# Kernel tuning notes

Hardware: AMD Instinct MI355X
Metric: run time of the kernel (lower is better)

The kernel has to match this reference:

```python
import jax, jax.numpy as jnp
import numpy as np

# ---- module config (from init_kwargs) ----
VOL_RANGE = np.array([-40.0, -40.0, -4.0, 40.0, 40.0, 4.0], np.float32)
VOXEL_SIZE = 0.4
GRID = tuple(int(v) for v in ((VOL_RANGE[3:] - VOL_RANGE[:3]) / VOXEL_SIZE).astype(np.int32))  # (200,200,20)
SIGMA_FACTOR = 3.0
OPACITY_THRESH = 1e-4
EPS = 1e-6
K = 8  # fixed local window per Gaussian (covers 3*sigma_max/voxel_size span)

B, N, C = 1, 25000, 8


def setup_inputs() -> dict:
    key = jax.random.key(0)
    k1, k2, k3, k4, k5 = jax.random.split(key, 5)
    lo = jnp.asarray(VOL_RANGE[:3]) + 1.0
    hi = jnp.asarray(VOL_RANGE[3:]) - 1.0
    means3d = lo + (hi - lo) * jax.random.uniform(k1, (B, N, 3), jnp.float32)
    opacities = jax.random.uniform(k2, (B, N, 1), jnp.float32)
    scales = 0.05 + 0.3 * jax.random.uniform(k3, (B, N, 3), jnp.float32)  # sigma_max=0.35m -> <=6 voxel span
    rotations = jax.random.normal(k4, (B, N, 4), jnp.float32)
    features = jax.random.normal(k5, (B, N, C), jnp.float32)
    return {"means3d": means3d, "opacities": opacities, "scales": scales,
            "rotations": rotations, "features": features}


def quat_scale_to_cov(scales, rotations):
    # matches CUDAVoxelizer._get_covariance
    q = rotations / jnp.sqrt(jnp.sum(rotations ** 2, -1, keepdims=True) + 1e-8)
    r, x, y, z = q[..., 0], q[..., 1], q[..., 2], q[..., 3]
    R = jnp.stack([
        1 - 2 * (y * y + z * z), 2 * (x * y - r * z), 2 * (x * z + r * y),
        2 * (x * y + r * z), 1 - 2 * (x * x + z * z), 2 * (y * z - r * x),
        2 * (x * z - r * y), 2 * (y * z + r * x), 1 - 2 * (x * x + y * y),
    ], axis=-1).reshape(q.shape[:-1] + (3, 3))
    L = R * scales[..., None, :]  # R @ diag(scales)
    return L @ jnp.swapaxes(L, -1, -2)


def voxelize_one(means, opac, cov, feats):
    """means [N,3], opac [N,1], cov [N,3,3], feats [N,C] -> density [X,Y,Z,1], gfeat [X,Y,Z,C]."""
    X, Y, Z = GRID
    V = X * Y * Z
    vol_min = jnp.asarray(VOL_RANGE[:3])
    vol_max = jnp.asarray(VOL_RANGE[3:])
    gmax = jnp.asarray(GRID, jnp.int32) - 1

    sigma = jnp.sqrt(jnp.diagonal(cov, axis1=-2, axis2=-1))          # [N,3]
    bmin = means - SIGMA_FACTOR * sigma
    bmax = means + SIGMA_FACTOR * sigma
    # _filter_gaussians_torch as a multiplicative mask (removed Gaussians contribute 0)
    keep = (jnp.all(bmax > vol_min, -1) & jnp.all(bmin < vol_max, -1)
            & (opac[:, 0] > OPACITY_THRESH))                          # [N]

    cov_inv = jnp.linalg.inv(cov)                                     # [N,3,3]
    bmin_s = jax.lax.stop_gradient(bmin)
    bmax_s = jax.lax.stop_gradient(bmax)
    # torch .int() truncates toward zero; clamp as in fallback
    idx_min = jnp.maximum(((bmin_s - vol_min) / VOXEL_SIZE).astype(jnp.int32), 0)     # [N,3]
    idx_max = jnp.minimum(((bmax_s - vol_min) / VOXEL_SIZE).astype(jnp.int32), gmax)  # [N,3]

    o = jnp.arange(K, dtype=jnp.int32)
    offs = jnp.stack(jnp.meshgrid(o, o, o, indexing='ij'), -1).reshape(-1, 3)  # [P,3], P=K^3
    vox = idx_min[:, None, :] + offs[None]                            # [N,P,3]
    valid = jnp.all(vox <= idx_max[:, None, :], -1)                   # [N,P]

    centers = vox.astype(jnp.float32) * VOXEL_SIZE + vol_min + 0.5 * VOXEL_SIZE
    diff = centers - means[:, None, :]                                # [N,P,3]
    maha = jnp.einsum('npi,nij,npj->np', diff, cov_inv, diff)
    contrib = opac * jnp.exp(-0.5 * maha)                             # [N,P] (opac [N,1] bcast)
    contrib = jnp.where(valid & keep[:, None], contrib, 0.0)

    flat = (vox[..., 0] * Y + vox[..., 1]) * Z + vox[..., 2]
    flat = jnp.clip(flat, 0, V - 1).reshape(-1)                       # zeroed contribs land harmlessly

    density = jnp.zeros((V,), jnp.float32).at[flat].add(contrib.reshape(-1))
    gfeat = jnp.zeros((V, C), jnp.float32).at[flat].add(
        (contrib[..., None] * feats[:, None, :]).reshape(-1, C))
    gfeat = gfeat / jnp.clip(density, EPS)[:, None]
    return density.reshape(X, Y, Z, 1), gfeat.reshape(X, Y, Z, C)


def reference(means3d, opacities, scales, rotations, features):
    cov = quat_scale_to_cov(scales.reshape(-1, 3), rotations.reshape(-1, 4))
    cov = cov.reshape(means3d.shape[0], -1, 3, 3)
    density, gfeat = jax.vmap(voxelize_one)(means3d, opacities, cov, features)
    return density, gfeat
```

## Files before the change

kernel.cpp:

```cpp
#include <hip/hip_runtime.h>

namespace {
constexpr int GX = 200, GY = 200, GZ = 20;
constexpr int NVOX = GX * GY * GZ;
constexpr float VMINX = -40.f, VMINY = -40.f, VMINZ = -4.f;
constexpr float VMAXX =  40.f, VMAXY =  40.f, VMAXZ =  4.f;
constexpr float VS    = 0.4f;
constexpr float HVS   = 0.2f;
constexpr float SIGF  = 3.0f;

constexpr int TILE   = 4;
constexpr int TX     = GX / TILE;
constexpr int TY     = GY / TILE;
constexpr int NTILES = TX * TY;
constexpr int CAP    = 128;
constexpr int PSTRIDE = 20;
}

__device__ __forceinline__ bool gauss_setup(
    const float* __restrict__ means, const float* __restrict__ opacs,
    const float* __restrict__ scales, const float* __restrict__ rots,
    int g,
    int& gx0, int& gx1, int& gy0, int& gy1, int& gz0, int& gz1,
    float& i00, float& i01, float& i02, float& i11, float& i12, float& i22,
    float& mx, float& my, float& mz, float& op)
{
    op = opacs[g];
    mx = means[3*g+0]; my = means[3*g+1]; mz = means[3*g+2];
    const float sx = scales[3*g+0], sy = scales[3*g+1], sz = scales[3*g+2];
    const float q0 = rots[4*g+0], q1 = rots[4*g+1], q2 = rots[4*g+2], q3 = rots[4*g+3];

    const float qn = sqrtf(q0*q0 + q1*q1 + q2*q2 + q3*q3 + 1e-8f);
    const float r = q0/qn, x = q1/qn, y = q2/qn, z = q3/qn;

    const float R00 = 1.f - 2.f*(y*y + z*z), R01 = 2.f*(x*y - r*z), R02 = 2.f*(x*z + r*y);
    const float R10 = 2.f*(x*y + r*z), R11 = 1.f - 2.f*(x*x + z*z), R12 = 2.f*(y*z - r*x);
    const float R20 = 2.f*(x*z - r*y), R21 = 2.f*(y*z + r*x), R22 = 1.f - 2.f*(x*x + y*y);

    const float s0 = sx*sx, s1 = sy*sy, s2 = sz*sz;
    const float c00 = R00*R00*s0 + R01*R01*s1 + R02*R02*s2;
    const float c01 = R00*R10*s0 + R01*R11*s1 + R02*R12*s2;
    const float c02 = R00*R20*s0 + R01*R21*s1 + R02*R22*s2;
    const float c11 = R10*R10*s0 + R11*R11*s1 + R12*R12*s2;
    const float c12 = R10*R20*s0 + R11*R21*s1 + R12*R22*s2;
    const float c22 = R20*R20*s0 + R21*R21*s1 + R22*R22*s2;

    const float sgx = SIGF * sqrtf(c00), sgy = SIGF * sqrtf(c11), sgz = SIGF * sqrtf(c22);
    const float bminx = mx - sgx, bminy = my - sgy, bminz = mz - sgz;
    const float bmaxx = mx + sgx, bmaxy = my + sgy, bmaxz = mz + sgz;

    const bool keep = (bmaxx > VMINX) && (bmaxy > VMINY) && (bmaxz > VMINZ)
                   && (bminx < VMAXX) && (bminy < VMAXY) && (bminz < VMAXZ)
                   && (op > 1e-4f);
    if (!keep) return false;

    gx0 = max((int)((bminx - VMINX) / VS), 0);
    gy0 = max((int)((bminy - VMINY) / VS), 0);
    gz0 = max((int)((bminz - VMINZ) / VS), 0);
    gx1 = min((int)((bmaxx - VMINX) / VS), GX - 1);
    gy1 = min((int)((bmaxy - VMINY) / VS), GY - 1);
    gz1 = min((int)((bmaxz - VMINZ) / VS), GZ - 1);
    gx1 = min(gx1, gx0 + 7);
    gy1 = min(gy1, gy0 + 7);
    gz1 = min(gz1, gz0 + 7);
    if (gx1 < gx0 || gy1 < gy0 || gz1 < gz0) return false;

    const float m00 = c11*c22 - c12*c12;
    const float m01 = c02*c12 - c01*c22;
    const float m02 = c01*c12 - c02*c11;
    const float det = c00*m00 + c01*m01 + c02*m02;
    const float id  = 1.f / det;
    i00 = m00*id; i01 = m01*id; i02 = m02*id;
    i11 = (c00*c22 - c02*c02)*id;
    i12 = (c01*c02 - c00*c12)*id;
    i22 = (c00*c11 - c01*c01)*id;
    return true;
}

__global__ __launch_bounds__(64) void voxel_bin(
    const float* __restrict__ means, const float* __restrict__ opacs,
    const float* __restrict__ scales, const float* __restrict__ rots,
    const float* __restrict__ feats,
    int* __restrict__ counts, int* __restrict__ entries,
    float* __restrict__ params, int N)
{
    const int g = blockIdx.x * blockDim.x + threadIdx.x;
    if (g >= N) return;
    int gx0, gx1, gy0, gy1, gz0, gz1;
    float i00,i01,i02,i11,i12,i22, mx,my,mz, op;
    if (!gauss_setup(means, opacs, scales, rots, g,
                     gx0,gx1,gy0,gy1,gz0,gz1, i00,i01,i02,i11,i12,i22, mx,my,mz, op))
        return;

    float* P = params + (size_t)g * PSTRIDE;
    const float4 f0 = *(const float4*)(feats + 8*g);
    const float4 f1 = *(const float4*)(feats + 8*g + 4);
    *(float4*)(P + 0)  = make_float4(i00, i01, i02, i11);
    *(float4*)(P + 4)  = make_float4(i12, i22, mx, my);
    *(float4*)(P + 8)  = make_float4(mz, op,
                                     __int_as_float(gx0 | (gy0<<8) | (gz0<<16)),
                                     __int_as_float(gx1 | (gy1<<8) | (gz1<<16)));
    *(float4*)(P + 12) = f0;
    *(float4*)(P + 16) = f1;

    const int tx0 = gx0 >> 2, tx1 = gx1 >> 2;
    const int ty0 = gy0 >> 2, ty1 = gy1 >> 2;
    for (int tx = tx0; tx <= tx1; ++tx)
        for (int ty = ty0; ty <= ty1; ++ty) {
            const int t = tx * TY + ty;
            const int slot = atomicAdd(&counts[t], 1);
            if (slot < CAP) entries[t * CAP + slot] = g;
        }
}

__global__ __launch_bounds__(64) void voxel_gather(
    const float* __restrict__ params,
    const int* __restrict__ counts, const int* __restrict__ entries,
    float* __restrict__ density, float* __restrict__ gfeat)
{
    __shared__ float gs[CAP][PSTRIDE];

    const int tile = blockIdx.x;
    const int ttx = tile / TY, tty = tile % TY;
    const int tid = threadIdx.x;
    const int cnt = min(counts[tile], CAP);

    for (int j = tid; j < cnt; j += 64) {
        const int g = entries[tile * CAP + j];
        const float* P = params + (size_t)g * PSTRIDE;
        float* G = gs[j];
        #pragma unroll
        for (int q = 0; q < 5; ++q)
            *(float4*)(G + 4*q) = *(const float4*)(P + 4*q);
    }
    __syncthreads();

    const int lx = tid & 3, ly = (tid >> 2) & 3, zs = (tid >> 4) * 5;
    const int vx = ttx * TILE + lx, vy = tty * TILE + ly;
    const float cx = (float)vx * VS + VMINX + HVS;
    const float cy = (float)vy * VS + VMINY + HVS;

    float den[5] = {0.f, 0.f, 0.f, 0.f, 0.f};
    float ft[5][8] = {};

    #pragma unroll 2
    for (int j = 0; j < cnt; ++j) {
        const float* G = gs[j];
        const int w0 = __float_as_int(G[10]);
        const int w1 = __float_as_int(G[11]);
        const int gx0 = w0 & 255, gy0 = (w0 >> 8) & 255, gz0 = (w0 >> 16) & 255;
        const int gx1 = w1 & 255, gy1 = (w1 >> 8) & 255, gz1 = (w1 >> 16) & 255;
        if (vx < gx0 || vx > gx1 || vy < gy0 || vy > gy1) continue;

        const float ddx = cx - G[6], ddy = cy - G[7];
        const float i00 = G[0], i01 = G[1], i02 = G[2];
        const float i11 = G[3], i12 = G[4], i22 = G[5];
        const float base = i00*ddx*ddx + 2.f*i01*ddx*ddy + i11*ddy*ddy;
        const float bz   = 2.f*(i02*ddx + i12*ddy);
        const float mz = G[8], op = G[9];
        const float f[8] = {G[12],G[13],G[14],G[15],G[16],G[17],G[18],G[19]};

        #pragma unroll
        for (int k = 0; k < 5; ++k) {
            const int vz = zs + k;
            if (vz < gz0 || vz > gz1) continue;
            const float ddz = ((float)vz * VS + VMINZ + HVS) - mz;
            const float w = op * __expf(-0.5f * (base + ddz * (bz + i22 * ddz)));
            den[k] += w;
            #pragma unroll
            for (int c = 0; c < 8; ++c) ft[k][c] += w * f[c];
        }
    }

    #pragma unroll
    for (int k = 0; k < 5; ++k) {
        const int vz = zs + k;
        const int flat = (vx * GY + vy) * GZ + vz;
        density[flat] = den[k];
        const float inv = 1.f / fmaxf(den[k], 1e-6f);
        float4 a = make_float4(ft[k][0]*inv, ft[k][1]*inv, ft[k][2]*inv, ft[k][3]*inv);
        float4 b = make_float4(ft[k][4]*inv, ft[k][5]*inv, ft[k][6]*inv, ft[k][7]*inv);
        *(float4*)(gfeat + (size_t)flat * 8)     = a;
        *(float4*)(gfeat + (size_t)flat * 8 + 4) = b;
    }
}

extern "C" void kernel_launch(void* const* d_in, const int* in_sizes, int n_in,
                              void* d_out, int out_size, void* d_ws, size_t ws_size,
                              hipStream_t stream)
{
    const float* means  = (const float*)d_in[0];
    const float* opacs  = (const float*)d_in[1];
    const float* scales = (const float*)d_in[2];
    const float* rots   = (const float*)d_in[3];
    const float* feats  = (const float*)d_in[4];

    float* density = (float*)d_out;
    float* gfeat   = density + NVOX;
    const int N = in_sizes[0] / 3;

    int*   counts  = (int*)d_ws;
    int*   entries = counts + NTILES;
    float* params  = (float*)(entries + NTILES * CAP);

    hipMemsetAsync(counts, 0, NTILES * sizeof(int), stream);

    voxel_bin<<<(N + 63) / 64, 64, 0, stream>>>(means, opacs, scales, rots, feats,
                                                counts, entries, params, N);
    voxel_gather<<<NTILES, 64, 0, stream>>>(params, counts, entries, density, gfeat);
}
```

Before: 109.7 us.

## Bin Gaussians into 3D 4x4x4 tiles and compute one voxel per thread

The 2D column tiles (4x4 xy, full z) become 4x4x4 voxel tiles split into 5 z segments, so each gather block only walks the Gaussians that overlap its z range. Each thread now handles a single voxel instead of 5 z voxels, which cuts registers and wasted iterations on Gaussians that miss the thread's z slice. The price is more atomics and entry writes in the binning pass, 5x more gather blocks and counts to clear, and a larger workspace. The per-Gaussian xy terms are no longer shared across several z voxels, so those terms are recomputed for every voxel.

```diff
diff --git a/kernel.cpp b/kernel.cpp
--- a/kernel.cpp
+++ b/kernel.cpp
@@ -10,9 +10,11 @@
 constexpr float SIGF  = 3.0f;
 
 constexpr int TILE   = 4;
+constexpr int ZSEG   = 4;
 constexpr int TX     = GX / TILE;
 constexpr int TY     = GY / TILE;
-constexpr int NTILES = TX * TY;
+constexpr int TZ     = GZ / ZSEG;
+constexpr int NTILES = TX * TY * TZ;
 constexpr int CAP    = 128;
 constexpr int PSTRIDE = 20;
 }
@@ -105,12 +107,14 @@
 
     const int tx0 = gx0 >> 2, tx1 = gx1 >> 2;
     const int ty0 = gy0 >> 2, ty1 = gy1 >> 2;
+    const int tz0 = gz0 >> 2, tz1 = gz1 >> 2;
     for (int tx = tx0; tx <= tx1; ++tx)
-        for (int ty = ty0; ty <= ty1; ++ty) {
-            const int t = tx * TY + ty;
-            const int slot = atomicAdd(&counts[t], 1);
-            if (slot < CAP) entries[t * CAP + slot] = g;
-        }
+        for (int ty = ty0; ty <= ty1; ++ty)
+            for (int tz = tz0; tz <= tz1; ++tz) {
+                const int t = (tx * TY + ty) * TZ + tz;
+                const int slot = atomicAdd(&counts[t], 1);
+                if (slot < CAP) entries[t * CAP + slot] = g;
+            }
 }
 
 __global__ __launch_bounds__(64) void voxel_gather(
@@ -121,9 +125,11 @@
     __shared__ float gs[CAP][PSTRIDE];
 
     const int tile = blockIdx.x;
-    const int ttx = tile / TY, tty = tile % TY;
-    const int tid = threadIdx.x;
-    const int cnt = min(counts[tile], CAP);
+    const int seg  = tile % TZ;
+    const int txy  = tile / TZ;
+    const int ttx  = txy / TY, tty = txy % TY;
+    const int tid  = threadIdx.x;
+    const int cnt  = min(counts[tile], CAP);
 
     for (int j = tid; j < cnt; j += 64) {
         const int g = entries[tile * CAP + j];
@@ -135,54 +141,41 @@
     }
     __syncthreads();
 
-    const int lx = tid & 3, ly = (tid >> 2) & 3, zs = (tid >> 4) * 5;
-    const int vx = ttx * TILE + lx, vy = tty * TILE + ly;
+    const int lz = tid & 3, ly = (tid >> 2) & 3, lx = tid >> 4;
+    const int vx = ttx * TILE + lx, vy = tty * TILE + ly, vz = seg * ZSEG + lz;
     const float cx = (float)vx * VS + VMINX + HVS;
     const float cy = (float)vy * VS + VMINY + HVS;
-
-    float den[5] = {0.f, 0.f, 0.f, 0.f, 0.f};
-    float ft[5][8] = {};
-
-    #pragma unroll 2
+    const float cz = (float)vz * VS + VMINZ + HVS;
+
+    float den = 0.f;
+    float ft0 = 0.f, ft1 = 0.f, ft2 = 0.f, ft3 = 0.f;
+    float ft4 = 0.f, ft5 = 0.f, ft6 = 0.f, ft7 = 0.f;
+
     for (int j = 0; j < cnt; ++j) {
         const float* G = gs[j];
         const int w0 = __float_as_int(G[10]);
         const int w1 = __float_as_int(G[11]);
         const int gx0 = w0 & 255, gy0 = (w0 >> 8) & 255, gz0 = (w0 >> 16) & 255;
         const int gx1 = w1 & 255, gy1 = (w1 >> 8) & 255, gz1 = (w1 >> 16) & 255;
-        if (vx < gx0 || vx > gx1 || vy < gy0 || vy > gy1) continue;
-
-        const float ddx = cx - G[6], ddy = cy - G[7];
-        const float i00 = G[0], i01 = G[1], i02 = G[2];
-        const float i11 = G[3], i12 = G[4], i22 = G[5];
-        const float base = i00*ddx*ddx + 2.f*i01*ddx*ddy + i11*ddy*ddy;
-        const float bz   = 2.f*(i02*ddx + i12*ddy);
-        const float mz = G[8], op = G[9];
-        const float f[8] = {G[12],G[13],G[14],G[15],G[16],G[17],G[18],G[19]};
-
-        #pragma unroll
-        for (int k = 0; k < 5; ++k) {
-            const int vz = zs + k;
-            if (vz < gz0 || vz > gz1) continue;
-            const float ddz = ((float)vz * VS + VMINZ + HVS) - mz;
-            const float w = op * __expf(-0.5f * (base + ddz * (bz + i22 * ddz)));
-            den[k] += w;
-            #pragma unroll
-            for (int c = 0; c < 8; ++c) ft[k][c] += w * f[c];
-        }
+        if (vx < gx0 || vx > gx1 || vy < gy0 || vy > gy1 || vz < gz0 || vz > gz1)
+            continue;
+
+        const float ddx = cx - G[6], ddy = cy - G[7], ddz = cz - G[8];
+        const float maha = G[0]*ddx*ddx + G[3]*ddy*ddy + G[5]*ddz*ddz
+                         + 2.f*(G[1]*ddx*ddy + G[2]*ddx*ddz + G[4]*ddy*ddz);
+        const float w = G[9] * __expf(-0.5f * maha);
+        den += w;
+        ft0 += w * G[12]; ft1 += w * G[13]; ft2 += w * G[14]; ft3 += w * G[15];
+        ft4 += w * G[16]; ft5 += w * G[17]; ft6 += w * G[18]; ft7 += w * G[19];
     }
 
-    #pragma unroll
-    for (int k = 0; k < 5; ++k) {
-        const int vz = zs + k;
-        const int flat = (vx * GY + vy) * GZ + vz;
-        density[flat] = den[k];
-        const float inv = 1.f / fmaxf(den[k], 1e-6f);
-        float4 a = make_float4(ft[k][0]*inv, ft[k][1]*inv, ft[k][2]*inv, ft[k][3]*inv);
-        float4 b = make_float4(ft[k][4]*inv, ft[k][5]*inv, ft[k][6]*inv, ft[k][7]*inv);
-        *(float4*)(gfeat + (size_t)flat * 8)     = a;
-        *(float4*)(gfeat + (size_t)flat * 8 + 4) = b;
-    }
+    const int flat = (vx * GY + vy) * GZ + vz;
+    density[flat] = den;
+    const float inv = 1.f / fmaxf(den, 1e-6f);
+    float4 a = make_float4(ft0*inv, ft1*inv, ft2*inv, ft3*inv);
+    float4 b = make_float4(ft4*inv, ft5*inv, ft6*inv, ft7*inv);
+    *(float4*)(gfeat + (size_t)flat * 8)     = a;
+    *(float4*)(gfeat + (size_t)flat * 8 + 4) = b;
 }
 
 extern "C" void kernel_launch(void* const* d_in, const int* in_sizes, int n_in,
@@ -201,7 +194,7 @@
 
     int*   counts  = (int*)d_ws;
     int*   entries = counts + NTILES;
-    float* params  = (float*)(entries + NTILES * CAP);
+    float* params  = (float*)(entries + (size_t)NTILES * CAP);
 
     hipMemsetAsync(counts, 0, NTILES * sizeof(int), stream);
 
```

Result: faster. 105.1 us (-4.2%).
